# Kernel tuning notes

Measured on AMD Instinct MI355X. Metric: run time of the kernel, lower is better.

Reference implementation:

```python
import jax, jax.numpy as jnp
import numpy as np

POOL_LEN = 256
EPS = 1e-5
WEIGHT_BITS = 2


def adaptive_avg_pool1d(x, out_len):
    """Faithful torch AdaptiveAvgPool1d: window i = [floor(i*L/out), ceil((i+1)*L/out)).
    Implemented via cumsum + static gathers (jit-friendly, vectorized)."""
    L = x.shape[-1]
    i = np.arange(out_len)
    starts = (i * L) // out_len
    ends = -((-(i + 1) * L) // out_len)  # integer ceil
    csum = jnp.cumsum(x, axis=-1)
    csum = jnp.concatenate([jnp.zeros(x.shape[:-1] + (1,), x.dtype), csum], axis=-1)
    counts = jnp.asarray(ends - starts, x.dtype)
    return (csum[..., ends] - csum[..., starts]) / counts


def quantize_weight(w, bits=WEIGHT_BITS):
    """2-bit symmetric uniform quantization, per-output-channel scale, STE."""
    qp = 2 ** (bits - 1) - 1          # +1
    qn = -(2 ** (bits - 1))           # -2
    scale = jnp.maximum(jnp.max(jnp.abs(w), axis=1, keepdims=True) / qp, 1e-8)
    w_q = jnp.clip(jnp.round(w / scale), qn, qp) * scale
    return w + jax.lax.stop_gradient(w_q - w)  # straight-through estimator


def setup_inputs() -> dict:
    key = jax.random.key(0)
    k1, k2, k3, kw = jax.random.split(key, 4)
    B = 64
    return {
        "stage1": jax.random.normal(k1, (B, 256, 5000), jnp.float32),
        "stage2": jax.random.normal(k2, (B, 128, 2500), jnp.float32),
        "stage3": jax.random.normal(k3, (B, 64, 625), jnp.float32),
        "alpha": jnp.ones((3,), jnp.float32) / 3.0,
        "weight": jax.random.normal(kw, (128, 448), jnp.float32) * 0.05,
        "bias": jnp.zeros((128,), jnp.float32),
        "gamma": jnp.ones((128,), jnp.float32),
        "beta": jnp.zeros((128,), jnp.float32),
    }


def reference(stage1, stage2, stage3, alpha, weight, bias, gamma, beta):
    w = jax.nn.softmax(alpha)
    s1 = adaptive_avg_pool1d(stage1, POOL_LEN) * w[0]
    s2 = adaptive_avg_pool1d(stage2, POOL_LEN) * w[1]
    s3 = adaptive_avg_pool1d(stage3, POOL_LEN) * w[2]
    fused = jnp.concatenate([s1, s2, s3], axis=1)  # (B, 448, 256)
    wq = quantize_weight(weight)
    y = jnp.einsum('oc,bcl->bol', wq, fused) + bias[None, :, None]  # (B, 128, 256)
    # BatchNorm1d (training mode: batch stats over N and L)
    mean = jnp.mean(y, axis=(0, 2))
    var = jnp.var(y, axis=(0, 2))
    yn = (y - mean[None, :, None]) * jax.lax.rsqrt(var + EPS)[None, :, None]
    yn = yn * gamma[None, :, None] + beta[None, :, None]
    act = jax.nn.elu(yn)
    return jnp.mean(act, axis=-1)  # (B, 128)
```

## Files before the change

### kernel.cpp

```cpp
#include <hip/hip_runtime.h>
#include <hip/hip_bf16.h>

#define EPSV 1e-5f

typedef __attribute__((ext_vector_type(8))) short short8v;
typedef __attribute__((ext_vector_type(4))) float float4v;

__device__ inline unsigned short f2bf(float x) {
  __hip_bfloat16 h = __float2bfloat16(x);
  return *reinterpret_cast<unsigned short*>(&h);
}
__device__ inline float bf2f(unsigned short b) {
  unsigned u = ((unsigned)b) << 16;
  float f;
  __builtin_memcpy(&f, &u, 4);
  return f;
}

__global__ __launch_bounds__(256) void pool_quant_kernel(
    const float* __restrict__ s1, const float* __restrict__ s2,
    const float* __restrict__ s3, const float* __restrict__ alpha,
    const float* __restrict__ w, unsigned short* __restrict__ fusedb,
    unsigned short* __restrict__ qbf, float* __restrict__ scales) {
  __shared__ float row[5000];
  int bid = blockIdx.x;
  int t = threadIdx.x;

  if (bid >= 28672) {
    int o = bid - 28672;
    const float* wr = w + o * 448;
    float m = 0.f;
    for (int c = t; c < 448; c += 256) m = fmaxf(m, fabsf(wr[c]));
    float* sm = row;
    for (int off = 32; off; off >>= 1) m = fmaxf(m, __shfl_down(m, off, 64));
    if ((t & 63) == 0) sm[t >> 6] = m;
    __syncthreads();
    m = fmaxf(fmaxf(sm[0], sm[1]), fmaxf(sm[2], sm[3]));
    float scale = fmaxf(m, 1e-8f);
    for (int c = t; c < 448; c += 256) {
      float q = rintf(wr[c] / scale);
      q = fminf(fmaxf(q, -2.f), 1.f);
      qbf[o * 448 + c] = f2bf(q);
    }
    if (t == 0) scales[o] = scale;
    return;
  }

  int b = bid / 448;
  int cg_ = bid % 448;
  const float* src; int C, L, c, widx;
  if (cg_ < 256)      { src = s1; C = 256; L = 5000; c = cg_;       widx = 0; }
  else if (cg_ < 384) { src = s2; C = 128; L = 2500; c = cg_ - 256; widx = 1; }
  else                { src = s3; C = 64;  L = 625;  c = cg_ - 384; widx = 2; }

  float a0 = alpha[0], a1 = alpha[1], a2 = alpha[2];
  float mx = fmaxf(a0, fmaxf(a1, a2));
  float e0 = expf(a0 - mx), e1 = expf(a1 - mx), e2 = expf(a2 - mx);
  float wst = ((widx == 0) ? e0 : (widx == 1) ? e1 : e2) / (e0 + e1 + e2);

  const float* rowp = src + ((size_t)b * C + c) * L;
  if ((L & 3) == 0) {
    const float4* rp4 = (const float4*)rowp;
    int L4 = L >> 2;
    for (int i = t; i < L4; i += 256) {
      float4 v = rp4[i];
      int j = i << 2;
      row[j] = v.x; row[j + 1] = v.y; row[j + 2] = v.z; row[j + 3] = v.w;
    }
  } else {
    for (int i = t; i < L; i += 256) row[i] = rowp[i];
  }
  __syncthreads();

  int l = t;
  int start = (l * L) >> 8;
  int end = ((l + 1) * L + 255) >> 8;
  float s = 0.f;
  for (int i = start; i < end; ++i) s += row[i];
  float v = s / (float)(end - start) * wst;
  fusedb[((size_t)b * 448 + cg_) * 256 + l] = f2bf(v);
}

__global__ __launch_bounds__(256) void mfma_gemm_kernel(
    const unsigned short* __restrict__ qbf, const float* __restrict__ scales,
    const unsigned short* __restrict__ fusedb, const float* __restrict__ bias,
    unsigned short* __restrict__ ybf, float* __restrict__ Psum,
    float* __restrict__ Pssq) {
  __shared__ __align__(16) unsigned short Asm[64][40];
  __shared__ __align__(16) unsigned short Bsm[32][66];
  int b = blockIdx.z;
  int o0 = blockIdx.y * 64;
  int l0 = blockIdx.x * 64;
  int tid = threadIdx.x;
  int wave = tid >> 6, lane = tid & 63;
  int wm = wave >> 1, wn = wave & 1;
  int lrow = lane & 15, lg = lane >> 4;
  const unsigned short* Fp = fusedb + (size_t)b * 448 * 256;
  float4v acc[2][2];
  #pragma unroll
  for (int i = 0; i < 2; ++i)
    #pragma unroll
    for (int j = 0; j < 2; ++j) acc[i][j] = (float4v){0.f, 0.f, 0.f, 0.f};
  for (int c0 = 0; c0 < 448; c0 += 32) {
    { int r = tid >> 2, k0 = (tid & 3) * 8;
      *(short8v*)&Asm[r][k0] = *(const short8v*)(qbf + (size_t)(o0 + r) * 448 + c0 + k0); }
    { int k = tid >> 3, n0 = (tid & 7) * 8;
      short8v v = *(const short8v*)(Fp + (size_t)(c0 + k) * 256 + l0 + n0);
      *(short8v*)&Bsm[k][n0] = v; }
    __syncthreads();
    short8v af[2];
    #pragma unroll
    for (int mf = 0; mf < 2; ++mf)
      af[mf] = *(const short8v*)&Asm[wm * 32 + mf * 16 + lrow][lg * 8];
    #pragma unroll
    for (int nf = 0; nf < 2; ++nf) {
      int n = wn * 32 + nf * 16 + lrow;
      short8v bf;
      #pragma unroll
      for (int j = 0; j < 8; ++j) bf[j] = (short)Bsm[lg * 8 + j][n];
      #pragma unroll
      for (int mf = 0; mf < 2; ++mf)
        acc[mf][nf] = __builtin_amdgcn_mfma_f32_16x16x32_bf16(af[mf], bf, acc[mf][nf], 0, 0, 0);
    }
    __syncthreads();
  }
  float sv[2][4], qv[2][4];
  #pragma unroll
  for (int mf = 0; mf < 2; ++mf) {
    #pragma unroll
    for (int reg = 0; reg < 4; ++reg) {
      int r = o0 + wm * 32 + mf * 16 + lg * 4 + reg;
      float sc = scales[r], bv = bias[r];
      float s = 0.f, q = 0.f;
      #pragma unroll
      for (int nf = 0; nf < 2; ++nf) {
        int col = l0 + wn * 32 + nf * 16 + lrow;
        float val = acc[mf][nf][reg] * sc + bv;
        ybf[((size_t)b * 128 + r) * 256 + col] = f2bf(val);
        s += val; q += val * val;
      }
      sv[mf][reg] = s; qv[mf][reg] = q;
    }
  }
  #pragma unroll
  for (int mf = 0; mf < 2; ++mf)
    #pragma unroll
    for (int reg = 0; reg < 4; ++reg)
      #pragma unroll
      for (int m = 1; m < 16; m <<= 1) {
        sv[mf][reg] += __shfl_xor(sv[mf][reg], m, 64);
        qv[mf][reg] += __shfl_xor(qv[mf][reg], m, 64);
      }
  if (lrow == 0) {
    int slot = b * 8 + blockIdx.x * 2 + wn;
    #pragma unroll
    for (int mf = 0; mf < 2; ++mf)
      #pragma unroll
      for (int reg = 0; reg < 4; ++reg) {
        int r = o0 + wm * 32 + mf * 16 + lg * 4 + reg;
        Psum[r * 512 + slot] = sv[mf][reg];
        Pssq[r * 512 + slot] = qv[mf][reg];
      }
  }
}

__global__ __launch_bounds__(256) void final_kernel(
    const unsigned short* __restrict__ ybf, const float* __restrict__ Psum,
    const float* __restrict__ Pssq, const float* __restrict__ gamma,
    const float* __restrict__ beta, float* __restrict__ out) {
  int w = threadIdx.x >> 6;
  int lane = threadIdx.x & 63;
  int bo = blockIdx.x * 4 + w;
  int o = bo & 127;

  float s = 0.f, q = 0.f;
  const float* Pp = Psum + o * 512 + lane * 8;
  const float* Qp = Pssq + o * 512 + lane * 8;
  #pragma unroll
  for (int i = 0; i < 8; ++i) { s += Pp[i]; q += Qp[i]; }
  #pragma unroll
  for (int m = 1; m < 64; m <<= 1) {
    s += __shfl_xor(s, m, 64);
    q += __shfl_xor(q, m, 64);
  }
  float mean = s * (1.f / 16384.f);
  float var = q * (1.f / 16384.f) - mean * mean;
  float rs = rsqrtf(var + EPSV);
  float a = rs * gamma[o];
  float bb = beta[o] - mean * a;

  ushort4 v = *(const ushort4*)(ybf + (size_t)bo * 256 + lane * 4);
  float acc = 0.f;
  #pragma unroll
  for (int j = 0; j < 4; ++j) {
    float e = bf2f((&v.x)[j]);
    float yn = e * a + bb;
    acc += yn > 0.f ? yn : expm1f(yn);
  }
  for (int m = 32; m; m >>= 1) acc += __shfl_down(acc, m, 64);
  if (lane == 0) out[bo] = acc * (1.f / 256.f);
}

extern "C" void kernel_launch(void* const* d_in, const int* in_sizes, int n_in,
                              void* d_out, int out_size, void* d_ws, size_t ws_size,
                              hipStream_t stream) {
  const float* s1     = (const float*)d_in[0];
  const float* s2     = (const float*)d_in[1];
  const float* s3     = (const float*)d_in[2];
  const float* alpha  = (const float*)d_in[3];
  const float* weight = (const float*)d_in[4];
  const float* bias   = (const float*)d_in[5];
  const float* gamma  = (const float*)d_in[6];
  const float* beta   = (const float*)d_in[7];
  float* out = (float*)d_out;

  char* ws = (char*)d_ws;
  unsigned short* fusedb = (unsigned short*)ws;
  unsigned short* qbf    = (unsigned short*)(ws + 14680064);
  float* scales          = (float*)(ws + 14794752);
  unsigned short* ybf    = (unsigned short*)(ws + 14795264);
  float* Psum            = (float*)(ws + 18989568);
  float* Pssq            = (float*)(ws + 19251712);

  pool_quant_kernel<<<28800, 256, 0, stream>>>(s1, s2, s3, alpha, weight,
                                               fusedb, qbf, scales);
  dim3 g(4, 2, 64);
  mfma_gemm_kernel<<<g, 256, 0, stream>>>(qbf, scales, fusedb, bias, ybf,
                                          Psum, Pssq);
  final_kernel<<<2048, 256, 0, stream>>>(ybf, Psum, Pssq, gamma, beta, out);
}
```

Baseline: 102.8 us.

## Pool one row-span per wavefront with nontemporal loads and pair-packed GEMM B tile

The pooling kernel now assigns one row span to each wavefront rather than one row per 256-thread block. Stage1 rows are split into two halves, and each wave stages its span in its own LDS slice using nontemporal float4 loads. It then sums fixed-width windows with masked unrolled loops, dropping the block-wide syncthreads and the serial variable-length loops. The GEMM B tile is repacked so each 32-bit LDS entry holds two adjacent-k bf16 values, which halves the LDS reads per MFMA operand. In exchange, more warps sit in a memory-bound kernel, and there is some leftover dead code in the start computation.

```diff
diff --git a/kernel.cpp b/kernel.cpp
--- a/kernel.cpp
+++ b/kernel.cpp
@@ -4,6 +4,7 @@
 #define EPSV 1e-5f
 
 typedef __attribute__((ext_vector_type(8))) short short8v;
+typedef __attribute__((ext_vector_type(4))) short short4v;
 typedef __attribute__((ext_vector_type(4))) float float4v;
 
 __device__ inline unsigned short f2bf(float x) {
@@ -17,21 +18,103 @@
   return f;
 }
 
+template <int L, int SPAN, int NOUT, int MAXW>
+__device__ __forceinline__ void pool_span_vec(
+    const float* __restrict__ spanp, int lbase, float wst,
+    unsigned short* __restrict__ outp,
+    float* __restrict__ seg, int lane) {
+  constexpr int S4 = SPAN / 4;
+  constexpr int NLD = (S4 + 63) / 64;
+  constexpr int OPL = NOUT / 64;
+  if (lane < MAXW + 3) seg[SPAN + lane] = 0.f;
+  const float4v* rp = (const float4v*)spanp;
+  #pragma unroll
+  for (int j = 0; j < NLD; ++j) {
+    int idx = lane + 64 * j;
+    if (NLD * 64 == S4 || idx < S4) {
+      float4v v = __builtin_nontemporal_load(rp + idx);
+      *(float4v*)&seg[idx * 4] = v;
+    }
+  }
+  constexpr int BASE_SHIFT = (L / SPAN == 2) ? 1 : 0;
+  unsigned short res[OPL];
+  #pragma unroll
+  for (int oo = 0; oo < OPL; ++oo) {
+    int l = lbase + lane * OPL + oo;
+    int start = ((l * L) >> 8) - ((lbase * L) >> 8 >> BASE_SHIFT << BASE_SHIFT);
+    int sbase = (lbase * L) >> 8;
+    start = ((l * L) >> 8) - sbase;
+    int end = (((l + 1) * L + 255) >> 8) - sbase;
+    int width = end - start;
+    float s = 0.f;
+    #pragma unroll
+    for (int i = 0; i < MAXW; ++i) {
+      float v = seg[start + i];
+      s += (i < width) ? v : 0.f;
+    }
+    res[oo] = f2bf(s / (float)width * wst);
+  }
+  if (OPL == 2) {
+    unsigned pk = ((unsigned)res[1] << 16) | res[0];
+    *(unsigned*)(outp + lane * 2) = pk;
+  } else {
+    unsigned pk0 = ((unsigned)res[1] << 16) | res[0];
+    unsigned pk1 = ((unsigned)res[3] << 16) | res[2];
+    unsigned long long pk = ((unsigned long long)pk1 << 32) | pk0;
+    *(unsigned long long*)(outp + lane * 4) = pk;
+  }
+}
+
+template <int L, int SPAN, int NOUT, int MAXW>
+__device__ __forceinline__ void pool_span_scalar(
+    const float* __restrict__ spanp, int lbase, float wst,
+    unsigned short* __restrict__ outp, float* __restrict__ seg, int lane) {
+  constexpr int NLD = (SPAN + 63) / 64;
+  constexpr int OPL = NOUT / 64;
+  if (lane < MAXW + 3) seg[SPAN + lane] = 0.f;
+  #pragma unroll
+  for (int j = 0; j < NLD; ++j) {
+    int idx = lane + 64 * j;
+    if (idx < SPAN) seg[idx] = __builtin_nontemporal_load(spanp + idx);
+  }
+  int sbase = (lbase * L) >> 8;
+  unsigned short res[OPL];
+  #pragma unroll
+  for (int oo = 0; oo < OPL; ++oo) {
+    int l = lbase + lane * OPL + oo;
+    int start = ((l * L) >> 8) - sbase;
+    int end = (((l + 1) * L + 255) >> 8) - sbase;
+    int width = end - start;
+    float s = 0.f;
+    #pragma unroll
+    for (int i = 0; i < MAXW; ++i) {
+      float v = seg[start + i];
+      s += (i < width) ? v : 0.f;
+    }
+    res[oo] = f2bf(s / (float)width * wst);
+  }
+  unsigned pk0 = ((unsigned)res[1] << 16) | res[0];
+  unsigned pk1 = ((unsigned)res[3] << 16) | res[2];
+  unsigned long long pk = ((unsigned long long)pk1 << 32) | pk0;
+  *(unsigned long long*)(outp + lane * 4) = pk;
+}
+
 __global__ __launch_bounds__(256) void pool_quant_kernel(
     const float* __restrict__ s1, const float* __restrict__ s2,
     const float* __restrict__ s3, const float* __restrict__ alpha,
     const float* __restrict__ w, unsigned short* __restrict__ fusedb,
     unsigned short* __restrict__ qbf, float* __restrict__ scales) {
-  __shared__ float row[5000];
+  __shared__ float pool_lds[4][2524];
   int bid = blockIdx.x;
   int t = threadIdx.x;
-
-  if (bid >= 28672) {
-    int o = bid - 28672;
+  int wv = t >> 6, lane = t & 63;
+
+  if (bid >= 11264) {
+    int o = bid - 11264;
     const float* wr = w + o * 448;
     float m = 0.f;
     for (int c = t; c < 448; c += 256) m = fmaxf(m, fabsf(wr[c]));
-    float* sm = row;
+    float* sm = pool_lds[0];
     for (int off = 32; off; off >>= 1) m = fmaxf(m, __shfl_down(m, off, 64));
     if ((t & 63) == 0) sm[t >> 6] = m;
     __syncthreads();
@@ -46,39 +129,32 @@
     return;
   }
 
-  int b = bid / 448;
-  int cg_ = bid % 448;
-  const float* src; int C, L, c, widx;
-  if (cg_ < 256)      { src = s1; C = 256; L = 5000; c = cg_;       widx = 0; }
-  else if (cg_ < 384) { src = s2; C = 128; L = 2500; c = cg_ - 256; widx = 1; }
-  else                { src = s3; C = 64;  L = 625;  c = cg_ - 384; widx = 2; }
-
   float a0 = alpha[0], a1 = alpha[1], a2 = alpha[2];
   float mx = fmaxf(a0, fmaxf(a1, a2));
   float e0 = expf(a0 - mx), e1 = expf(a1 - mx), e2 = expf(a2 - mx);
-  float wst = ((widx == 0) ? e0 : (widx == 1) ? e1 : e2) / (e0 + e1 + e2);
-
-  const float* rowp = src + ((size_t)b * C + c) * L;
-  if ((L & 3) == 0) {
-    const float4* rp4 = (const float4*)rowp;
-    int L4 = L >> 2;
-    for (int i = t; i < L4; i += 256) {
-      float4 v = rp4[i];
-      int j = i << 2;
-      row[j] = v.x; row[j + 1] = v.y; row[j + 2] = v.z; row[j + 3] = v.w;
-    }
+  float esum = e0 + e1 + e2;
+  float* seg = pool_lds[wv];
+
+  if (bid < 8192) {
+    int u = bid * 4 + wv;
+    int rr = u >> 1, h = u & 1;
+    int b = rr >> 8, c = rr & 255;
+    const float* spanp = s1 + ((size_t)b * 256 + c) * 5000 + h * 2500;
+    unsigned short* outp = fusedb + ((size_t)b * 448 + c) * 256 + h * 128;
+    pool_span_vec<5000, 2500, 128, 21>(spanp, h * 128, e0 / esum, outp, seg, lane);
+  } else if (bid < 10240) {
+    int u = (bid - 8192) * 4 + wv;
+    int b = u >> 7, c = u & 127;
+    const float* spanp = s2 + ((size_t)b * 128 + c) * 2500;
+    unsigned short* outp = fusedb + ((size_t)b * 448 + 256 + c) * 256;
+    pool_span_vec<2500, 2500, 256, 11>(spanp, 0, e1 / esum, outp, seg, lane);
   } else {
-    for (int i = t; i < L; i += 256) row[i] = rowp[i];
-  }
-  __syncthreads();
-
-  int l = t;
-  int start = (l * L) >> 8;
-  int end = ((l + 1) * L + 255) >> 8;
-  float s = 0.f;
-  for (int i = start; i < end; ++i) s += row[i];
-  float v = s / (float)(end - start) * wst;
-  fusedb[((size_t)b * 448 + cg_) * 256 + l] = f2bf(v);
+    int u = (bid - 10240) * 4 + wv;
+    int b = u >> 6, c = u & 63;
+    const float* spanp = s3 + ((size_t)b * 64 + c) * 625;
+    unsigned short* outp = fusedb + ((size_t)b * 448 + 384 + c) * 256;
+    pool_span_scalar<625, 625, 256, 4>(spanp, 0, e2 / esum, outp, seg, lane);
+  }
 }
 
 __global__ __launch_bounds__(256) void mfma_gemm_kernel(
@@ -87,7 +163,7 @@
     unsigned short* __restrict__ ybf, float* __restrict__ Psum,
     float* __restrict__ Pssq) {
   __shared__ __align__(16) unsigned short Asm[64][40];
-  __shared__ __align__(16) unsigned short Bsm[32][66];
+  __shared__ __align__(16) unsigned Bsm32[16][66];
   int b = blockIdx.z;
   int o0 = blockIdx.y * 64;
   int l0 = blockIdx.x * 64;
@@ -104,9 +180,15 @@
   for (int c0 = 0; c0 < 448; c0 += 32) {
     { int r = tid >> 2, k0 = (tid & 3) * 8;
       *(short8v*)&Asm[r][k0] = *(const short8v*)(qbf + (size_t)(o0 + r) * 448 + c0 + k0); }
-    { int k = tid >> 3, n0 = (tid & 7) * 8;
-      short8v v = *(const short8v*)(Fp + (size_t)(c0 + k) * 256 + l0 + n0);
-      *(short8v*)&Bsm[k][n0] = v; }
+    { int kp = tid >> 4, n0 = (tid & 15) * 4;
+      const unsigned short* g0 = Fp + (size_t)(c0 + 2 * kp) * 256 + l0 + n0;
+      short4v v0 = *(const short4v*)g0;
+      short4v v1 = *(const short4v*)(g0 + 256);
+      #pragma unroll
+      for (int j = 0; j < 4; ++j)
+        Bsm32[kp][n0 + j] =
+            (((unsigned)(unsigned short)v1[j]) << 16) | (unsigned short)v0[j];
+    }
     __syncthreads();
     short8v af[2];
     #pragma unroll
@@ -115,9 +197,11 @@
     #pragma unroll
     for (int nf = 0; nf < 2; ++nf) {
       int n = wn * 32 + nf * 16 + lrow;
+      int tmp[4];
+      #pragma unroll
+      for (int jj = 0; jj < 4; ++jj) tmp[jj] = (int)Bsm32[lg * 4 + jj][n];
       short8v bf;
-      #pragma unroll
-      for (int j = 0; j < 8; ++j) bf[j] = (short)Bsm[lg * 8 + j][n];
+      __builtin_memcpy(&bf, tmp, 16);
       #pragma unroll
       for (int mf = 0; mf < 2; ++mf)
         acc[mf][nf] = __builtin_amdgcn_mfma_f32_16x16x32_bf16(af[mf], bf, acc[mf][nf], 0, 0, 0);
@@ -222,7 +306,7 @@
   float* Psum            = (float*)(ws + 18989568);
   float* Pssq            = (float*)(ws + 19251712);
 
-  pool_quant_kernel<<<28800, 256, 0, stream>>>(s1, s2, s3, alpha, weight,
+  pool_quant_kernel<<<11392, 256, 0, stream>>>(s1, s2, s3, alpha, weight,
                                                fusedb, qbf, scales);
   dim3 g(4, 2, 64);
   mfma_gemm_kernel<<<g, 256, 0, stream>>>(qbf, scales, fusedb, bias, ybf,
```

After: 93.16 us. 1.1x faster.
